# Performance work log

Hardware: AMD Instinct MI355X
Metric: run time of the kernel (lower is better)

## Reference

```python
import jax, jax.numpy as jnp
import numpy as np

N_NODES = 100000
N_EDGES = 1600000
D_IN = 128
D_OUT = 32
DROP_P = 0.6
NEG_SLOPE = 0.2


def setup_inputs() -> dict:
    key = jax.random.key(0)
    ks = jax.random.split(key, 10)
    x = jax.random.normal(ks[0], (N_NODES, D_IN), dtype=jnp.float32)
    edge_index = jax.random.randint(ks[1], (2, N_EDGES), 0, N_NODES, dtype=jnp.int32)
    drop_u = jax.random.uniform(ks[2], (N_NODES, D_IN), dtype=jnp.float32)
    s = 1.0 / np.sqrt(D_IN)
    W_src = jax.random.normal(ks[3], (D_IN, D_OUT), dtype=jnp.float32) * s
    W_dst = jax.random.normal(ks[4], (D_IN, D_OUT), dtype=jnp.float32) * s
    att_src = jax.random.normal(ks[5], (D_OUT,), dtype=jnp.float32) * s
    att_dst = jax.random.normal(ks[6], (D_OUT,), dtype=jnp.float32) * s
    bias_gat = jax.random.normal(ks[7], (D_OUT,), dtype=jnp.float32) * 0.01
    W_lin = jax.random.normal(ks[8], (D_OUT, D_OUT), dtype=jnp.float32) / np.sqrt(D_OUT)
    b_lin = jax.random.normal(ks[9], (D_OUT,), dtype=jnp.float32) * 0.01
    return {"x": x, "edge_index": edge_index, "drop_u": drop_u,
            "W_src": W_src, "W_dst": W_dst, "att_src": att_src,
            "att_dst": att_dst, "bias_gat": bias_gat,
            "W_lin": W_lin, "b_lin": b_lin}


def reference(x, edge_index, drop_u, W_src, W_dst, att_src, att_dst,
              bias_gat, W_lin, b_lin):
    n = x.shape[0]
    # F.dropout(x, p=0.6, training=True) with deterministic uniform draws
    keep = (drop_u > DROP_P).astype(x.dtype)
    xd = x * keep / (1.0 - DROP_P)

    # GATConv (heads=1): separate src/dst linear maps
    h_src = xd @ W_src                      # [N, D_OUT]
    h_dst = xd @ W_dst                      # [N, D_OUT]
    a_src = h_src @ att_src                 # [N]
    a_dst = h_dst @ att_dst                 # [N]

    # add_self_loops=True (PyG default)
    loops = jnp.arange(n, dtype=edge_index.dtype)
    src = jnp.concatenate([edge_index[0], loops])   # [E+N]
    dst = jnp.concatenate([edge_index[1], loops])   # [E+N]

    e = a_src[src] + a_dst[dst]                      # per-edge raw score
    e = jnp.where(e > 0, e, NEG_SLOPE * e)           # leaky_relu(0.2)

    # segment softmax over destination-node neighborhoods
    e_max = jax.ops.segment_max(e, dst, num_segments=n)  # every node has a self loop
    e_exp = jnp.exp(e - e_max[dst])
    denom = jax.ops.segment_sum(e_exp, dst, num_segments=n)
    alpha = e_exp / denom[dst]                       # [E+N]

    # scatter-add aggregation of weighted source features
    msg = h_src[src] * alpha[:, None]                # [E+N, D_OUT]
    out = jax.ops.segment_sum(msg, dst, num_segments=n) + bias_gat

    # residual linear + relu + log_softmax
    out = out + out @ W_lin + b_lin
    out = jax.nn.relu(out)
    logp = jax.nn.log_softmax(out, axis=1)
    return logp, alpha
```

## Files before the change

kernel.cpp:

```cpp
#include <hip/hip_runtime.h>
#include <math.h>

#define D_IN   128
#define D_OUT  32
#define NEG_SLOPE 0.2f
#define DROP_P 0.6f
#define KEEP_SCALE 2.5f

#define NPB     128
#define NB      782
#define CAPB    2816
#define CHUNK   4096
#define BT      512
#define EPT     8
#define SRC_BITS 17
#define SRC_MASK ((1u << SRC_BITS) - 1)

#define SLICES  4
#define NPS     32
#define CAPS    896
#define EPT3    11

#define WT_LD   (D_IN + 4)

__device__ __forceinline__ void atomicMaxF(float* addr, float v) {
    if (v >= 0.0f) atomicMax((int*)addr, __float_as_int(v));
    else           atomicMin((unsigned int*)addr, __float_as_uint(v));
}

__global__ void k_fold(const float* __restrict__ W_src, const float* __restrict__ W_dst,
                       const float* __restrict__ att_src, const float* __restrict__ att_dst,
                       float* __restrict__ v_src, float* __restrict__ v_dst,
                       int* __restrict__ gcur) {
    int gi = blockIdx.x * blockDim.x + threadIdx.x;
    if (gi < NB) gcur[gi] = gi * CAPB;
    if (blockIdx.x == 0) {
        int k = threadIdx.x;
        if (k < D_IN) {
            float s = 0.f, d = 0.f;
            #pragma unroll
            for (int c = 0; c < D_OUT; ++c) {
                s += W_src[k * D_OUT + c] * att_src[c];
                d += W_dst[k * D_OUT + c] * att_dst[c];
            }
            v_src[k] = s;
            v_dst[k] = d;
        }
    }
}

__global__ __launch_bounds__(256) void k_nodes(
    const float* __restrict__ x, const float* __restrict__ drop_u,
    const float* __restrict__ W_src,
    const float* __restrict__ v_src, const float* __restrict__ v_dst,
    float* __restrict__ h_src, float* __restrict__ a_src, float* __restrict__ a_dst,
    float* __restrict__ e_max, float* __restrict__ denom,
    float* __restrict__ agg, int n, int init_aux)
{
    __shared__ float WT[D_OUT][WT_LD];
    __shared__ float xdl[8][D_IN];
    __shared__ float vs[D_IN], vd[D_IN];

    int tid = threadIdx.x;
    for (int i = tid; i < D_IN * D_OUT; i += 256) {
        int k = i >> 5, c = i & 31;
        WT[c][k] = W_src[i];
    }
    if (tid < D_IN) { vs[tid] = v_src[tid]; vd[tid] = v_dst[tid]; }
    __syncthreads();

    int loc  = tid >> 5;
    int lane = tid & 31;
    int node = blockIdx.x * 8 + loc;

    if (node < n) {
        const float4* xr = (const float4*)(x      + (size_t)node * D_IN);
        const float4* dr = (const float4*)(drop_u + (size_t)node * D_IN);
        float4 xv = xr[lane];
        float4 dv = dr[lane];
        float4 xd4;
        xd4.x = dv.x > DROP_P ? xv.x * KEEP_SCALE : 0.f;
        xd4.y = dv.y > DROP_P ? xv.y * KEEP_SCALE : 0.f;
        xd4.z = dv.z > DROP_P ? xv.z * KEEP_SCALE : 0.f;
        xd4.w = dv.w > DROP_P ? xv.w * KEEP_SCALE : 0.f;
        ((float4*)xdl[loc])[lane] = xd4;

        int kb = lane * 4;
        float ps = xd4.x * vs[kb] + xd4.y * vs[kb + 1] + xd4.z * vs[kb + 2] + xd4.w * vs[kb + 3];
        float pd = xd4.x * vd[kb] + xd4.y * vd[kb + 1] + xd4.z * vd[kb + 2] + xd4.w * vd[kb + 3];
        #pragma unroll
        for (int off = 16; off; off >>= 1) {
            ps += __shfl_xor(ps, off);
            pd += __shfl_xor(pd, off);
        }
        if (lane == 0) {
            a_src[node] = ps;
            a_dst[node] = pd;
            if (init_aux) { e_max[node] = -3.0e38f; denom[node] = 0.f; }
        }
    }
    __syncthreads();

    if (node < n) {
        const float4* xr4 = (const float4*)xdl[loc];
        float acc = 0.f;
        #pragma unroll 8
        for (int kb = 0; kb < 32; ++kb) {
            float4 xb = xr4[kb];
            float4 w  = *(const float4*)&WT[lane][kb * 4];
            acc += xb.x * w.x + xb.y * w.y + xb.z * w.z + xb.w * w.w;
        }
        h_src[(size_t)node * D_OUT + lane] = acc;
        if (init_aux) agg[(size_t)node * D_OUT + lane] = 0.f;
    }
}

__global__ __launch_bounds__(BT) void k_binsort(
    const int* __restrict__ ei, int E, int n,
    int* __restrict__ gcur, unsigned* __restrict__ binned)
{
    __shared__ int A[1024], B[1024];
    __shared__ int excl[NB + 1];
    __shared__ int lcur[NB];
    __shared__ int gpos[NB];
    __shared__ unsigned stage[CHUNK];
    __shared__ unsigned short sbk[CHUNK];

    int tid = threadIdx.x;
    int T   = E + n;
    int base = blockIdx.x * CHUNK;

    for (int k = tid; k < 1024; k += BT) A[k] = 0;
    __syncthreads();

    unsigned rec[EPT];
    int      bk [EPT];
    #pragma unroll
    for (int e = 0; e < EPT; ++e) {
        int i = base + e * BT + tid;
        if (i < T) {
            int s, d;
            if (i < E) { s = ei[i]; d = ei[E + i]; }
            else       { s = d = i - E; }
            int b    = d >> 7;
            int drel = d & 127;
            rec[e] = (unsigned)s | ((unsigned)drel << SRC_BITS);
            bk[e]  = b;
            atomicAdd(&A[b], 1);
        } else bk[e] = -1;
    }
    __syncthreads();

    int* cur = A; int* nxt = B;
    for (int off = 1; off < 1024; off <<= 1) {
        for (int k = tid; k < 1024; k += BT) {
            int v = cur[k];
            if (k >= off) v += cur[k - off];
            nxt[k] = v;
        }
        __syncthreads();
        int* t = cur; cur = nxt; nxt = t;
    }

    for (int b = tid; b < NB; b += BT) {
        int e0 = b ? cur[b - 1] : 0;
        excl[b] = e0;
        lcur[b] = e0;
        int c = cur[b] - e0;
        gpos[b] = c ? atomicAdd(&gcur[b], c) : 0;
    }
    if (tid == 0) excl[NB] = cur[NB - 1];
    __syncthreads();

    #pragma unroll
    for (int e = 0; e < EPT; ++e) {
        if (bk[e] >= 0) {
            int slot = atomicAdd(&lcur[bk[e]], 1);
            stage[slot] = rec[e];
            sbk[slot]   = (unsigned short)bk[e];
        }
    }
    __syncthreads();

    int tot = excl[NB];
    for (int j = tid; j < tot; j += BT) {
        int b = sbk[j];
        unsigned gd = (unsigned)(gpos[b] + (j - excl[b]));
        if (gd < (unsigned)(b + 1) * CAPB)
            binned[gd] = stage[j];
    }
}

__global__ __launch_bounds__(256) void k_bucket3(
    const unsigned* __restrict__ binned, const int* __restrict__ gcur,
    const float* __restrict__ a_src, const float* __restrict__ a_dst,
    const float* __restrict__ h_src,
    const float* __restrict__ bias_gat, const float* __restrict__ W_lin,
    const float* __restrict__ b_lin,
    float* __restrict__ inv_out,
    float* __restrict__ io, int n)
{
    __shared__ unsigned grp_e[CAPS];
    __shared__ float    ex[CAPS];
    __shared__ int A[NPS];
    __shared__ int ends[NPS];
    __shared__ int ncur[NPS];
    __shared__ float Wl[D_OUT * D_OUT];
    __shared__ float ul[8][D_OUT];

    int tid   = threadIdx.x;
    int b     = blockIdx.x >> 2;
    int slice = blockIdx.x & 3;
    int n0    = b * NPB + slice * NPS;
    int nn    = n - n0; if (nn > NPS) nn = NPS;
    if (nn <= 0) return;

    for (int i = tid; i < D_OUT * D_OUT; i += 256) Wl[i] = W_lin[i];
    if (tid < NPS) A[tid] = 0;
    __syncthreads();

    int cnt = gcur[b] - b * CAPB;
    if (cnt > CAPB) cnt = CAPB;
    const unsigned* src = binned + (size_t)b * CAPB;

    unsigned rr[EPT3];
    #pragma unroll
    for (int e = 0; e < EPT3; ++e) {
        int j = tid + e * 256;
        if (j < cnt) {
            unsigned r = src[j];
            rr[e] = r;
            int drel = r >> SRC_BITS;
            if ((drel >> 5) == slice) atomicAdd(&A[drel & 31], 1);
        }
    }
    __syncthreads();

    if (tid < NPS) {
        int v = A[tid];
        #pragma unroll
        for (int off = 1; off < NPS; off <<= 1) {
            int u = __shfl_up(v, off, NPS);
            if (tid >= off) v += u;
        }
        ends[tid] = v;
        ncur[tid] = v - A[tid];
    }
    __syncthreads();

    #pragma unroll
    for (int e = 0; e < EPT3; ++e) {
        int j = tid + e * 256;
        if (j < cnt) {
            unsigned r = rr[e];
            int drel = r >> SRC_BITS;
            if ((drel >> 5) == slice) {
                int pos = atomicAdd(&ncur[drel & 31], 1);
                if (pos < CAPS) grp_e[pos] = r;
            }
        }
    }
    __syncthreads();

    int g = tid >> 5, lane = tid & 31;
    float bg = bias_gat[lane];
    float bl = b_lin[lane];

    for (int nr = g; nr < nn; nr += 8) {
        int st = nr ? ends[nr - 1] : 0;
        int en = ends[nr];
        if (st > CAPS) st = CAPS;
        if (en > CAPS) en = CAPS;
        int node = n0 + nr;
        float adst = a_dst[node];

        float ss = 0.f;
        for (int j = st + lane; j < en; j += 32) {
            float e = a_src[grp_e[j] & SRC_MASK] + adst;
            e = e > 0.f ? e : NEG_SLOPE * e;
            float v = expf(e);
            ex[j] = v;
            ss += v;
        }
        #pragma unroll
        for (int o = 16; o; o >>= 1) ss += __shfl_xor(ss, o);
        float inv = 1.0f / ss;
        if (lane == 0) inv_out[node] = inv;

        float acc0 = 0.f, acc1 = 0.f, acc2 = 0.f, acc3 = 0.f;
        int j = st;
        for (; j + 3 < en; j += 4) {
            unsigned r0 = grp_e[j], r1 = grp_e[j + 1], r2 = grp_e[j + 2], r3 = grp_e[j + 3];
            acc0 += h_src[((r0 & SRC_MASK) << 5) + lane] * ex[j];
            acc1 += h_src[((r1 & SRC_MASK) << 5) + lane] * ex[j + 1];
            acc2 += h_src[((r2 & SRC_MASK) << 5) + lane] * ex[j + 2];
            acc3 += h_src[((r3 & SRC_MASK) << 5) + lane] * ex[j + 3];
        }
        for (; j < en; ++j)
            acc0 += h_src[((grp_e[j] & SRC_MASK) << 5) + lane] * ex[j];

        float u = ((acc0 + acc1) + (acc2 + acc3)) * inv + bg;
        ul[g][lane] = u;
        float r2 = u + bl;
        #pragma unroll 8
        for (int k = 0; k < D_OUT; ++k)
            r2 += ul[g][k] * Wl[k * D_OUT + lane];
        r2 = fmaxf(r2, 0.f);

        float mm = r2;
        #pragma unroll
        for (int o = 16; o; o >>= 1) mm = fmaxf(mm, __shfl_xor(mm, o));
        float e2 = expf(r2 - mm);
        float s2 = e2;
        #pragma unroll
        for (int o = 16; o; o >>= 1) s2 += __shfl_xor(s2, o);
        io[(size_t)node * D_OUT + lane] = r2 - mm - logf(s2);
    }
}

__global__ void k_alpha(const int* __restrict__ ei, int E, int n,
                        const float* __restrict__ a_src, const float* __restrict__ a_dst,
                        const float* __restrict__ inv,
                        float* __restrict__ alpha_out)
{
    int i = blockIdx.x * blockDim.x + threadIdx.x;
    int T = E + n;
    if (i >= T) return;
    int s, d;
    if (i < E) { s = ei[i]; d = ei[E + i]; }
    else       { s = d = i - E; }
    float e = a_src[s] + a_dst[d];
    e = e > 0.f ? e : NEG_SLOPE * e;
    alpha_out[i] = expf(e) * inv[d];
}

__global__ void k_edge_score(const int* __restrict__ ei, int E, int n,
                             const float* __restrict__ a_src, const float* __restrict__ a_dst,
                             float* __restrict__ score_out, float* __restrict__ e_max)
{
    int total = E + n;
    int i = blockIdx.x * blockDim.x + threadIdx.x;
    if (i >= total) return;
    int s, d;
    if (i < E) { s = ei[i]; d = ei[E + i]; }
    else       { s = d = i - E; }
    float e = a_src[s] + a_dst[d];
    e = e > 0.f ? e : NEG_SLOPE * e;
    score_out[i] = e;
    atomicMaxF(&e_max[d], e);
}

__global__ void k_edge_exp(const int* __restrict__ ei, int E, int n,
                           const float* __restrict__ e_max,
                           float* __restrict__ score_io, float* __restrict__ denom)
{
    int total = E + n;
    int i = blockIdx.x * blockDim.x + threadIdx.x;
    if (i >= total) return;
    int d = (i < E) ? ei[E + i] : (i - E);
    float ex = expf(score_io[i] - e_max[d]);
    score_io[i] = ex;
    atomicAdd(&denom[d], ex);
}

__global__ __launch_bounds__(256) void k_edge_agg(
    const int* __restrict__ ei, int E, int n,
    const float* __restrict__ h_src, const float* __restrict__ denom,
    float* __restrict__ alpha_io, float* __restrict__ agg)
{
    int tid  = threadIdx.x;
    int loc  = tid >> 5;
    int lane = tid & 31;
    int i = blockIdx.x * 8 + loc;
    int total = E + n;
    if (i >= total) return;
    int s, d;
    if (i < E) { s = ei[i]; d = ei[E + i]; }
    else       { s = d = i - E; }
    float alpha = alpha_io[i] / denom[d];
    if (lane == 0) alpha_io[i] = alpha;
    float m = h_src[(size_t)s * D_OUT + lane] * alpha;
    atomicAdd(&agg[(size_t)d * D_OUT + lane], m);
}

__global__ __launch_bounds__(256) void k_final(
    const float* __restrict__ bias_gat, const float* __restrict__ W_lin,
    const float* __restrict__ b_lin, float* __restrict__ io, int n)
{
    __shared__ float Wl[D_OUT * D_OUT];
    __shared__ float ul[8][D_OUT];

    int tid = threadIdx.x;
    for (int i = tid; i < D_OUT * D_OUT; i += 256) Wl[i] = W_lin[i];
    __syncthreads();

    int loc  = tid >> 5;
    int lane = tid & 31;
    int node = blockIdx.x * 8 + loc;

    float u = 0.f;
    if (node < n) u = io[(size_t)node * D_OUT + lane] + bias_gat[lane];
    ul[loc][lane] = u;
    __syncthreads();

    float r = u + b_lin[lane];
    #pragma unroll 8
    for (int k = 0; k < D_OUT; ++k)
        r += ul[loc][k] * Wl[k * D_OUT + lane];
    r = fmaxf(r, 0.f);

    float m = r;
    #pragma unroll
    for (int off = 16; off; off >>= 1) m = fmaxf(m, __shfl_xor(m, off));
    float ex = expf(r - m);
    float ssum = ex;
    #pragma unroll
    for (int off = 16; off; off >>= 1) ssum += __shfl_xor(ssum, off);
    float logp = r - m - logf(ssum);

    if (node < n) io[(size_t)node * D_OUT + lane] = logp;
}

extern "C" void kernel_launch(void* const* d_in, const int* in_sizes, int n_in,
                              void* d_out, int out_size, void* d_ws, size_t ws_size,
                              hipStream_t stream)
{
    const float* x        = (const float*)d_in[0];
    const int*   ei       = (const int*)  d_in[1];
    const float* drop_u   = (const float*)d_in[2];
    const float* W_src    = (const float*)d_in[3];
    const float* W_dst    = (const float*)d_in[4];
    const float* att_src  = (const float*)d_in[5];
    const float* att_dst  = (const float*)d_in[6];
    const float* bias_gat = (const float*)d_in[7];
    const float* W_lin    = (const float*)d_in[8];
    const float* b_lin    = (const float*)d_in[9];

    const int N = in_sizes[0] / D_IN;
    const int E = in_sizes[1] / 2;
    const int total = E + N;

    float* ws = (float*)d_ws;

    float* v_src = ws;
    float* v_dst = ws + 128;
    float* h_src = ws + 256;
    float* a_src = h_src + (size_t)N * D_OUT;
    float* a_dst = a_src + N;
    float* m_buf = a_dst + N;
    float* i_buf = m_buf + N;

    size_t idx = 256 + (size_t)N * D_OUT + 4 * (size_t)N;
    int* gcur = (int*)(ws + idx);       idx += NB + 2;
    unsigned* binned = (unsigned*)(ws + idx); idx += (size_t)NB * CAPB;
    size_t need_bytes = idx * sizeof(float);

    float* logp_out  = (float*)d_out;
    float* alpha_out = (float*)d_out + (size_t)N * D_OUT;

    int nodeBlocks = (N + 7) / 8;
    int eb = (total + 255) / 256;

    bool fits = (ws_size >= need_bytes) && (N < (1 << SRC_BITS)) && (N <= NB * NPB);

    if (fits) {
        k_fold<<<(NB + 127) / 128, 128, 0, stream>>>(W_src, W_dst, att_src, att_dst,
                                                     v_src, v_dst, gcur);
        k_nodes<<<nodeBlocks, 256, 0, stream>>>(x, drop_u, W_src, v_src, v_dst,
                                                h_src, a_src, a_dst,
                                                nullptr, nullptr, nullptr, N, 0);
        int nchunk = (total + CHUNK - 1) / CHUNK;
        k_binsort<<<nchunk, BT, 0, stream>>>(ei, E, N, gcur, binned);
        k_bucket3<<<NB * SLICES, 256, 0, stream>>>(binned, gcur, a_src, a_dst, h_src,
                                                   bias_gat, W_lin, b_lin,
                                                   i_buf, logp_out, N);
        k_alpha<<<eb, 256, 0, stream>>>(ei, E, N, a_src, a_dst, i_buf, alpha_out);
    } else {
        k_fold<<<(NB + 127) / 128, 128, 0, stream>>>(W_src, W_dst, att_src, att_dst,
                                                     v_src, v_dst, gcur);
        k_nodes<<<nodeBlocks, 256, 0, stream>>>(x, drop_u, W_src, v_src, v_dst,
                                                h_src, a_src, a_dst,
                                                m_buf, i_buf, logp_out, N, 1);
        k_edge_score<<<eb, 256, 0, stream>>>(ei, E, N, a_src, a_dst, alpha_out, m_buf);
        k_edge_exp<<<eb, 256, 0, stream>>>(ei, E, N, m_buf, alpha_out, i_buf);
        int aggBlocks = (total + 7) / 8;
        k_edge_agg<<<aggBlocks, 256, 0, stream>>>(ei, E, N, h_src, i_buf, alpha_out, logp_out);
        k_final<<<nodeBlocks, 256, 0, stream>>>(bias_gat, W_lin, b_lin, logp_out, N);
    }
}
```

Before: 152.0 us.

## Process 32 nodes per block in k_nodes with 4-node register tiling

k_nodes now handles 32 nodes per block instead of 8. Each warp-sized group computes four nodes' h_src outputs at once, so each W column read from shared memory is reused across four nodes, and the transposed W load is spread over fewer blocks. The dropout staging loop is cooperative across the whole block, and the padded xdl rows avoid bank conflicts. In exchange there are four times fewer blocks, more registers per thread and a larger shared footprint. k_final keeps its old 8-node grid.

```diff
diff --git a/kernel.cpp b/kernel.cpp
--- a/kernel.cpp
+++ b/kernel.cpp
@@ -22,6 +22,7 @@
 #define EPT3    11
 
 #define WT_LD   (D_IN + 4)
+#define NPBK    32
 
 __device__ __forceinline__ void atomicMaxF(float* addr, float v) {
     if (v >= 0.0f) atomicMax((int*)addr, __float_as_int(v));
@@ -58,7 +59,7 @@
     float* __restrict__ agg, int n, int init_aux)
 {
     __shared__ float WT[D_OUT][WT_LD];
-    __shared__ float xdl[8][D_IN];
+    __shared__ float xdl[NPBK][WT_LD];
     __shared__ float vs[D_IN], vd[D_IN];
 
     int tid = threadIdx.x;
@@ -67,51 +68,70 @@
         WT[c][k] = W_src[i];
     }
     if (tid < D_IN) { vs[tid] = v_src[tid]; vd[tid] = v_dst[tid]; }
-    __syncthreads();
-
-    int loc  = tid >> 5;
-    int lane = tid & 31;
-    int node = blockIdx.x * 8 + loc;
-
-    if (node < n) {
-        const float4* xr = (const float4*)(x      + (size_t)node * D_IN);
-        const float4* dr = (const float4*)(drop_u + (size_t)node * D_IN);
-        float4 xv = xr[lane];
-        float4 dv = dr[lane];
-        float4 xd4;
-        xd4.x = dv.x > DROP_P ? xv.x * KEEP_SCALE : 0.f;
-        xd4.y = dv.y > DROP_P ? xv.y * KEEP_SCALE : 0.f;
-        xd4.z = dv.z > DROP_P ? xv.z * KEEP_SCALE : 0.f;
-        xd4.w = dv.w > DROP_P ? xv.w * KEEP_SCALE : 0.f;
-        ((float4*)xdl[loc])[lane] = xd4;
-
-        int kb = lane * 4;
-        float ps = xd4.x * vs[kb] + xd4.y * vs[kb + 1] + xd4.z * vs[kb + 2] + xd4.w * vs[kb + 3];
-        float pd = xd4.x * vd[kb] + xd4.y * vd[kb + 1] + xd4.z * vd[kb + 2] + xd4.w * vd[kb + 3];
-        #pragma unroll
-        for (int off = 16; off; off >>= 1) {
-            ps += __shfl_xor(ps, off);
-            pd += __shfl_xor(pd, off);
-        }
-        if (lane == 0) {
-            a_src[node] = ps;
-            a_dst[node] = pd;
-            if (init_aux) { e_max[node] = -3.0e38f; denom[node] = 0.f; }
-        }
-    }
-    __syncthreads();
-
-    if (node < n) {
-        const float4* xr4 = (const float4*)xdl[loc];
-        float acc = 0.f;
-        #pragma unroll 8
-        for (int kb = 0; kb < 32; ++kb) {
-            float4 xb = xr4[kb];
-            float4 w  = *(const float4*)&WT[lane][kb * 4];
-            acc += xb.x * w.x + xb.y * w.y + xb.z * w.z + xb.w * w.w;
-        }
-        h_src[(size_t)node * D_OUT + lane] = acc;
-        if (init_aux) agg[(size_t)node * D_OUT + lane] = 0.f;
+
+    int n0 = blockIdx.x * NPBK;
+
+    for (int idx = tid; idx < NPBK * 32; idx += 256) {
+        int nl = idx >> 5, l4 = idx & 31;
+        int node = n0 + nl;
+        if (node < n) {
+            float4 xv = ((const float4*)(x      + (size_t)node * D_IN))[l4];
+            float4 dv = ((const float4*)(drop_u + (size_t)node * D_IN))[l4];
+            float4 xd4;
+            xd4.x = dv.x > DROP_P ? xv.x * KEEP_SCALE : 0.f;
+            xd4.y = dv.y > DROP_P ? xv.y * KEEP_SCALE : 0.f;
+            xd4.z = dv.z > DROP_P ? xv.z * KEEP_SCALE : 0.f;
+            xd4.w = dv.w > DROP_P ? xv.w * KEEP_SCALE : 0.f;
+            *(float4*)&xdl[nl][l4 * 4] = xd4;
+        }
+    }
+    __syncthreads();
+
+    int g = tid >> 5, lane = tid & 31;
+    int nb4 = g * 4;
+
+    #pragma unroll
+    for (int i = 0; i < 4; ++i) {
+        int node = n0 + nb4 + i;
+        if (node < n) {
+            float4 xd4 = *(const float4*)&xdl[nb4 + i][lane * 4];
+            int kb = lane * 4;
+            float ps = xd4.x * vs[kb] + xd4.y * vs[kb + 1] + xd4.z * vs[kb + 2] + xd4.w * vs[kb + 3];
+            float pd = xd4.x * vd[kb] + xd4.y * vd[kb + 1] + xd4.z * vd[kb + 2] + xd4.w * vd[kb + 3];
+            #pragma unroll
+            for (int off = 16; off; off >>= 1) {
+                ps += __shfl_xor(ps, off);
+                pd += __shfl_xor(pd, off);
+            }
+            if (lane == 0) {
+                a_src[node] = ps;
+                a_dst[node] = pd;
+                if (init_aux) { e_max[node] = -3.0e38f; denom[node] = 0.f; }
+            }
+        }
+    }
+
+    float acc0 = 0.f, acc1 = 0.f, acc2 = 0.f, acc3 = 0.f;
+    #pragma unroll 8
+    for (int kb = 0; kb < 32; ++kb) {
+        float4 w  = *(const float4*)&WT[lane][kb * 4];
+        float4 xa = *(const float4*)&xdl[nb4 + 0][kb * 4];
+        float4 xb = *(const float4*)&xdl[nb4 + 1][kb * 4];
+        float4 xc = *(const float4*)&xdl[nb4 + 2][kb * 4];
+        float4 xd = *(const float4*)&xdl[nb4 + 3][kb * 4];
+        acc0 += xa.x * w.x + xa.y * w.y + xa.z * w.z + xa.w * w.w;
+        acc1 += xb.x * w.x + xb.y * w.y + xb.z * w.z + xb.w * w.w;
+        acc2 += xc.x * w.x + xc.y * w.y + xc.z * w.z + xc.w * w.w;
+        acc3 += xd.x * w.x + xd.y * w.y + xd.z * w.z + xd.w * w.w;
+    }
+    float accs[4] = {acc0, acc1, acc2, acc3};
+    #pragma unroll
+    for (int i = 0; i < 4; ++i) {
+        int node = n0 + nb4 + i;
+        if (node < n) {
+            h_src[(size_t)node * D_OUT + lane] = accs[i];
+            if (init_aux) agg[(size_t)node * D_OUT + lane] = 0.f;
+        }
     }
 }
 
@@ -458,7 +478,8 @@
     float* logp_out  = (float*)d_out;
     float* alpha_out = (float*)d_out + (size_t)N * D_OUT;
 
-    int nodeBlocks = (N + 7) / 8;
+    int nodeBlocks = (N + NPBK - 1) / NPBK;
+    int nodeBlocks8 = (N + 7) / 8;
     int eb = (total + 255) / 256;
 
     bool fits = (ws_size >= need_bytes) && (N < (1 << SRC_BITS)) && (N <= NB * NPB);
@@ -485,6 +506,6 @@
         k_edge_exp<<<eb, 256, 0, stream>>>(ei, E, N, m_buf, alpha_out, i_buf);
         int aggBlocks = (total + 7) / 8;
         k_edge_agg<<<aggBlocks, 256, 0, stream>>>(ei, E, N, h_src, i_buf, alpha_out, logp_out);
-        k_final<<<nodeBlocks, 256, 0, stream>>>(bias_gat, W_lin, b_lin, logp_out, N);
-    }
-}
+        k_final<<<nodeBlocks8, 256, 0, stream>>>(bias_gat, W_lin, b_lin, logp_out, N);
+    }
+}
```

Result: no change. 152.6 us (+0.4%).

## Remap node projection to one thread per node with register-resident rows

Applied to the files above, without the earlier changes.

Rewrites k_nodes so each thread handles a whole node instead of a 32-lane group per node. The dropout-scaled input row is held in registers, and W_src is read from LDS as broadcast float4 loads, which removes the shared staging buffer, the shuffle reductions and one barrier. The block size drops to 64 threads. In exchange, each lane now reads its own 512-byte row, so global loads are strided rather than coalesced. The 128-float register array also raises register pressure and may lower occupancy. The fallback k_final launch keeps its old grid size.

```diff
diff --git a/kernel.cpp b/kernel.cpp
--- a/kernel.cpp
+++ b/kernel.cpp
@@ -20,8 +20,6 @@
 #define NPS     32
 #define CAPS    896
 #define EPT3    11
-
-#define WT_LD   (D_IN + 4)
 
 __device__ __forceinline__ void atomicMaxF(float* addr, float v) {
     if (v >= 0.0f) atomicMax((int*)addr, __float_as_int(v));
@@ -49,7 +47,7 @@
     }
 }
 
-__global__ __launch_bounds__(256) void k_nodes(
+__global__ __launch_bounds__(64) void k_nodes(
     const float* __restrict__ x, const float* __restrict__ drop_u,
     const float* __restrict__ W_src,
     const float* __restrict__ v_src, const float* __restrict__ v_dst,
@@ -57,61 +55,68 @@
     float* __restrict__ e_max, float* __restrict__ denom,
     float* __restrict__ agg, int n, int init_aux)
 {
-    __shared__ float WT[D_OUT][WT_LD];
-    __shared__ float xdl[8][D_IN];
-    __shared__ float vs[D_IN], vd[D_IN];
+    __shared__ float WT[D_OUT][D_IN];
+    __shared__ float vsl[D_IN], vdl[D_IN];
 
     int tid = threadIdx.x;
-    for (int i = tid; i < D_IN * D_OUT; i += 256) {
+    for (int i = tid; i < D_IN * D_OUT; i += 64) {
         int k = i >> 5, c = i & 31;
         WT[c][k] = W_src[i];
     }
-    if (tid < D_IN) { vs[tid] = v_src[tid]; vd[tid] = v_dst[tid]; }
-    __syncthreads();
-
-    int loc  = tid >> 5;
-    int lane = tid & 31;
-    int node = blockIdx.x * 8 + loc;
-
-    if (node < n) {
-        const float4* xr = (const float4*)(x      + (size_t)node * D_IN);
-        const float4* dr = (const float4*)(drop_u + (size_t)node * D_IN);
-        float4 xv = xr[lane];
-        float4 dv = dr[lane];
-        float4 xd4;
-        xd4.x = dv.x > DROP_P ? xv.x * KEEP_SCALE : 0.f;
-        xd4.y = dv.y > DROP_P ? xv.y * KEEP_SCALE : 0.f;
-        xd4.z = dv.z > DROP_P ? xv.z * KEEP_SCALE : 0.f;
-        xd4.w = dv.w > DROP_P ? xv.w * KEEP_SCALE : 0.f;
-        ((float4*)xdl[loc])[lane] = xd4;
-
-        int kb = lane * 4;
-        float ps = xd4.x * vs[kb] + xd4.y * vs[kb + 1] + xd4.z * vs[kb + 2] + xd4.w * vs[kb + 3];
-        float pd = xd4.x * vd[kb] + xd4.y * vd[kb + 1] + xd4.z * vd[kb + 2] + xd4.w * vd[kb + 3];
-        #pragma unroll
-        for (int off = 16; off; off >>= 1) {
-            ps += __shfl_xor(ps, off);
-            pd += __shfl_xor(pd, off);
-        }
-        if (lane == 0) {
-            a_src[node] = ps;
-            a_dst[node] = pd;
-            if (init_aux) { e_max[node] = -3.0e38f; denom[node] = 0.f; }
-        }
-    }
-    __syncthreads();
-
-    if (node < n) {
-        const float4* xr4 = (const float4*)xdl[loc];
-        float acc = 0.f;
-        #pragma unroll 8
+    for (int i = tid; i < D_IN; i += 64) { vsl[i] = v_src[i]; vdl[i] = v_dst[i]; }
+    __syncthreads();
+
+    int node_raw = blockIdx.x * 64 + tid;
+    bool act = node_raw < n;
+    int node = act ? node_raw : (n - 1);
+
+    const float4* xr4 = (const float4*)(x      + (size_t)node * D_IN);
+    const float4* dr4 = (const float4*)(drop_u + (size_t)node * D_IN);
+
+    float4 xr[32];
+    float ps = 0.f, pd = 0.f;
+    #pragma unroll
+    for (int kb = 0; kb < 32; ++kb) {
+        float4 xv = xr4[kb];
+        float4 dv = dr4[kb];
+        float4 v;
+        v.x = dv.x > DROP_P ? xv.x * KEEP_SCALE : 0.f;
+        v.y = dv.y > DROP_P ? xv.y * KEEP_SCALE : 0.f;
+        v.z = dv.z > DROP_P ? xv.z * KEEP_SCALE : 0.f;
+        v.w = dv.w > DROP_P ? xv.w * KEEP_SCALE : 0.f;
+        xr[kb] = v;
+        float4 vs4 = *(const float4*)&vsl[kb * 4];
+        float4 vd4 = *(const float4*)&vdl[kb * 4];
+        ps += v.x * vs4.x + v.y * vs4.y + v.z * vs4.z + v.w * vs4.w;
+        pd += v.x * vd4.x + v.y * vd4.y + v.z * vd4.z + v.w * vd4.w;
+    }
+    if (act) {
+        a_src[node] = ps;
+        a_dst[node] = pd;
+        if (init_aux) { e_max[node] = -3.0e38f; denom[node] = 0.f; }
+    }
+
+    size_t hbase = (size_t)node * D_OUT;
+    for (int cg = 0; cg < 4; ++cg) {
+        float acc[8];
+        #pragma unroll
+        for (int ci = 0; ci < 8; ++ci) acc[ci] = 0.f;
+        #pragma unroll
         for (int kb = 0; kb < 32; ++kb) {
-            float4 xb = xr4[kb];
-            float4 w  = *(const float4*)&WT[lane][kb * 4];
-            acc += xb.x * w.x + xb.y * w.y + xb.z * w.z + xb.w * w.w;
-        }
-        h_src[(size_t)node * D_OUT + lane] = acc;
-        if (init_aux) agg[(size_t)node * D_OUT + lane] = 0.f;
+            float4 xv = xr[kb];
+            #pragma unroll
+            for (int ci = 0; ci < 8; ++ci) {
+                float4 w = *(const float4*)&WT[cg * 8 + ci][kb * 4];
+                acc[ci] += xv.x * w.x + xv.y * w.y + xv.z * w.z + xv.w * w.w;
+            }
+        }
+        if (act) {
+            #pragma unroll
+            for (int ci = 0; ci < 8; ++ci) {
+                h_src[hbase + cg * 8 + ci] = acc[ci];
+                if (init_aux) agg[hbase + cg * 8 + ci] = 0.f;
+            }
+        }
     }
 }
 
@@ -458,7 +463,8 @@
     float* logp_out  = (float*)d_out;
     float* alpha_out = (float*)d_out + (size_t)N * D_OUT;
 
-    int nodeBlocks = (N + 7) / 8;
+    int nodeBlocks = (N + 63) / 64;
+    int nodeBlocks8 = (N + 7) / 8;
     int eb = (total + 255) / 256;
 
     bool fits = (ws_size >= need_bytes) && (N < (1 << SRC_BITS)) && (N <= NB * NPB);
@@ -466,9 +472,9 @@
     if (fits) {
         k_fold<<<(NB + 127) / 128, 128, 0, stream>>>(W_src, W_dst, att_src, att_dst,
                                                      v_src, v_dst, gcur);
-        k_nodes<<<nodeBlocks, 256, 0, stream>>>(x, drop_u, W_src, v_src, v_dst,
-                                                h_src, a_src, a_dst,
-                                                nullptr, nullptr, nullptr, N, 0);
+        k_nodes<<<nodeBlocks, 64, 0, stream>>>(x, drop_u, W_src, v_src, v_dst,
+                                               h_src, a_src, a_dst,
+                                               nullptr, nullptr, nullptr, N, 0);
         int nchunk = (total + CHUNK - 1) / CHUNK;
         k_binsort<<<nchunk, BT, 0, stream>>>(ei, E, N, gcur, binned);
         k_bucket3<<<NB * SLICES, 256, 0, stream>>>(binned, gcur, a_src, a_dst, h_src,
@@ -478,13 +484,13 @@
     } else {
         k_fold<<<(NB + 127) / 128, 128, 0, stream>>>(W_src, W_dst, att_src, att_dst,
                                                      v_src, v_dst, gcur);
-        k_nodes<<<nodeBlocks, 256, 0, stream>>>(x, drop_u, W_src, v_src, v_dst,
-                                                h_src, a_src, a_dst,
-                                                m_buf, i_buf, logp_out, N, 1);
+        k_nodes<<<nodeBlocks, 64, 0, stream>>>(x, drop_u, W_src, v_src, v_dst,
+                                               h_src, a_src, a_dst,
+                                               m_buf, i_buf, logp_out, N, 1);
         k_edge_score<<<eb, 256, 0, stream>>>(ei, E, N, a_src, a_dst, alpha_out, m_buf);
         k_edge_exp<<<eb, 256, 0, stream>>>(ei, E, N, m_buf, alpha_out, i_buf);
         int aggBlocks = (total + 7) / 8;
         k_edge_agg<<<aggBlocks, 256, 0, stream>>>(ei, E, N, h_src, i_buf, alpha_out, logp_out);
-        k_final<<<nodeBlocks, 256, 0, stream>>>(bias_gat, W_lin, b_lin, logp_out, N);
-    }
-}
+        k_final<<<nodeBlocks8, 256, 0, stream>>>(bias_gat, W_lin, b_lin, logp_out, N);
+    }
+}
```

Result: slower. 478.3 us (+214.7%).
